# Kernel tuning notes

Hardware: AMD Instinct MI355X
Metric: run time of the kernel (lower is better)

## Reference

```python
import jax, jax.numpy as jnp
import numpy as np

def setup_inputs() -> dict:
    key = jax.random.key(0)
    k1, k2 = jax.random.split(key)
    B, T = 256, 100000
    x = jax.random.normal(k1, (B, T), dtype=jnp.float32)
    shifts = jax.random.randint(k2, (B,), 0, 1000, dtype=jnp.int32)
    return {"x": x, "shifts": shifts}

def reference(x, shifts):
    # tf.roll(x[i], shift=s, axis=0): out[j] = x[(j - s) % T]
    B, T = x.shape
    idx = (jnp.arange(T, dtype=jnp.int32)[None, :] - shifts[:, None]) % T  # [B, T]
    return jnp.take_along_axis(x, idx, axis=1)
```

## Files before the change

kernel.cpp:

```cpp
#include <hip/hip_runtime.h>

__global__ void roll_rows_vec4(const float* __restrict__ x,
                               const int* __restrict__ shifts,
                               float* __restrict__ out,
                               int T, int T4) {
    const int b = blockIdx.y;
    const int v = blockIdx.x * blockDim.x + threadIdx.x;
    if (v >= T4) return;

    int s = shifts[b] % T;
    if (s < 0) s += T;

    const int j = v * 4;
    int i0 = j - s;
    if (i0 < 0) i0 += T;

    const float* __restrict__ xr = x + (size_t)b * (size_t)T;
    float4 r;
    if (i0 + 3 < T) {
        r.x = xr[i0];
        r.y = xr[i0 + 1];
        r.z = xr[i0 + 2];
        r.w = xr[i0 + 3];
    } else {
        int i1 = i0 + 1; if (i1 >= T) i1 -= T;
        int i2 = i0 + 2; if (i2 >= T) i2 -= T;
        int i3 = i0 + 3; if (i3 >= T) i3 -= T;
        r.x = xr[i0];
        r.y = xr[i1];
        r.z = xr[i2];
        r.w = xr[i3];
    }
    *reinterpret_cast<float4*>(out + (size_t)b * (size_t)T + j) = r;
}

__global__ void roll_rows_scalar(const float* __restrict__ x,
                                 const int* __restrict__ shifts,
                                 float* __restrict__ out,
                                 int T) {
    const int b = blockIdx.y;
    const int j = blockIdx.x * blockDim.x + threadIdx.x;
    if (j >= T) return;
    int s = shifts[b] % T;
    if (s < 0) s += T;
    int i = j - s;
    if (i < 0) i += T;
    out[(size_t)b * T + j] = x[(size_t)b * T + i];
}

extern "C" void kernel_launch(void* const* d_in, const int* in_sizes, int n_in,
                              void* d_out, int out_size, void* d_ws, size_t ws_size,
                              hipStream_t stream) {
    const float* x = (const float*)d_in[0];
    const int* shifts = (const int*)d_in[1];
    float* out = (float*)d_out;

    const int B = in_sizes[1];
    const int T = in_sizes[0] / B;

    if ((T & 3) == 0) {
        const int T4 = T / 4;
        dim3 block(256);
        dim3 grid((T4 + 255) / 256, B);
        roll_rows_vec4<<<grid, block, 0, stream>>>(x, shifts, out, T, T4);
    } else {
        dim3 block(256);
        dim3 grid((T + 255) / 256, B);
        roll_rows_scalar<<<grid, block, 0, stream>>>(x, shifts, out, T);
    }
}
```

Baseline: 174.6 us.

## Stage rolled rows through padded LDS to use aligned float4 global loads

Replaces the per-thread scalar unaligned gathers with a block-level scheme. Each block reads an aligned span of the source row with float4 loads into padded shared memory, then reads it back at the shift offset and writes float4 outputs. The goal is fewer, wider global load transactions. In exchange it adds an LDS round trip and a barrier, and its correctness depends on T being a multiple of 4 so that the wrapped aligned loads stay in bounds.

```diff
diff --git a/kernel.cpp b/kernel.cpp
--- a/kernel.cpp
+++ b/kernel.cpp
@@ -1,37 +1,55 @@
 #include <hip/hip_runtime.h>
 
-__global__ void roll_rows_vec4(const float* __restrict__ x,
-                               const int* __restrict__ shifts,
-                               float* __restrict__ out,
-                               int T, int T4) {
+
+#define CHUNK 1024
+
+__device__ __forceinline__ int pad(int i) { return i + (i >> 2); }
+
+__global__ __launch_bounds__(256) void roll_rows_lds(
+    const float* __restrict__ x,
+    const int* __restrict__ shifts,
+    float* __restrict__ out,
+    int T) {
+    __shared__ float lds[CHUNK + 4 + ((CHUNK + 4) >> 2) + 4];
+
     const int b = blockIdx.y;
-    const int v = blockIdx.x * blockDim.x + threadIdx.x;
-    if (v >= T4) return;
+    const int chunk0 = blockIdx.x * CHUNK;
+    const int t = threadIdx.x;
 
     int s = shifts[b] % T;
     if (s < 0) s += T;
 
-    const int j = v * 4;
-    int i0 = j - s;
-    if (i0 < 0) i0 += T;
+    const int nOut = min(CHUNK, T - chunk0);
+    const int base = chunk0 - s;
+    const int off = ((base % 4) + 4) % 4;
+    const int baseAl = base - off;
+    const int nV = (nOut + off + 3) >> 2;
 
     const float* __restrict__ xr = x + (size_t)b * (size_t)T;
-    float4 r;
-    if (i0 + 3 < T) {
-        r.x = xr[i0];
-        r.y = xr[i0 + 1];
-        r.z = xr[i0 + 2];
-        r.w = xr[i0 + 3];
-    } else {
-        int i1 = i0 + 1; if (i1 >= T) i1 -= T;
-        int i2 = i0 + 2; if (i2 >= T) i2 -= T;
-        int i3 = i0 + 3; if (i3 >= T) i3 -= T;
-        r.x = xr[i0];
-        r.y = xr[i1];
-        r.z = xr[i2];
-        r.w = xr[i3];
+
+    for (int k = t; k < nV; k += 256) {
+        int src = baseAl + 4 * k;
+        if (src < 0) src += T;
+        else if (src >= T) src -= T;
+        const float4 v = *reinterpret_cast<const float4*>(xr + src);
+        const int i = 4 * k;
+        lds[pad(i + 0)] = v.x;
+        lds[pad(i + 1)] = v.y;
+        lds[pad(i + 2)] = v.z;
+        lds[pad(i + 3)] = v.w;
     }
-    *reinterpret_cast<float4*>(out + (size_t)b * (size_t)T + j) = r;
+    __syncthreads();
+
+    const int j = 4 * t;
+    if (j < nOut) {
+        const int i = off + j;
+        float4 o;
+        o.x = lds[pad(i + 0)];
+        o.y = lds[pad(i + 1)];
+        o.z = lds[pad(i + 2)];
+        o.w = lds[pad(i + 3)];
+        *reinterpret_cast<float4*>(out + (size_t)b * (size_t)T + chunk0 + j) = o;
+    }
 }
 
 __global__ void roll_rows_scalar(const float* __restrict__ x,
@@ -59,10 +77,9 @@
     const int T = in_sizes[0] / B;
 
     if ((T & 3) == 0) {
-        const int T4 = T / 4;
         dim3 block(256);
-        dim3 grid((T4 + 255) / 256, B);
-        roll_rows_vec4<<<grid, block, 0, stream>>>(x, shifts, out, T, T4);
+        dim3 grid((T + CHUNK - 1) / CHUNK, B);
+        roll_rows_lds<<<grid, block, 0, stream>>>(x, shifts, out, T);
     } else {
         dim3 block(256);
         dim3 grid((T + 255) / 256, B);
```

Result: no change. 177.8 us (+1.8%).

## Use aligned float4 loads with wavefront shuffle realignment for row roll

Applied to the files above, without the earlier changes.

Replaces the per-thread unaligned scalar gathers with a wave-per-chunk scheme. Each row is split into 32 spans, and each wavefront loads aligned float4 vectors. The misaligned offset is fixed with __shfl_down across lanes, so every lane writes a full float4 and 63 of 64 lanes store 252 floats per iteration. The change is meant to cut load instruction count and uncoalesced traffic on a bandwidth-bound copy. It adds shuffle overhead and one idle lane per wave, and it relies on blocks = B*32/4 dividing evenly.

```diff
diff --git a/kernel.cpp b/kernel.cpp
--- a/kernel.cpp
+++ b/kernel.cpp
@@ -1,37 +1,79 @@
 #include <hip/hip_runtime.h>
 
-__global__ void roll_rows_vec4(const float* __restrict__ x,
-                               const int* __restrict__ shifts,
-                               float* __restrict__ out,
-                               int T, int T4) {
-    const int b = blockIdx.y;
-    const int v = blockIdx.x * blockDim.x + threadIdx.x;
-    if (v >= T4) return;
 
-    int s = shifts[b] % T;
+#define WPR 32
+
+__global__ __launch_bounds__(256) void roll_rows_funnel(
+    const float* __restrict__ x,
+    const int* __restrict__ shifts,
+    float* __restrict__ out,
+    int T, int span) {
+    const int tid = blockIdx.x * 256 + threadIdx.x;
+    const int w = tid >> 6;
+    const int L = threadIdx.x & 63;
+    const int r = w / WPR;
+    const int k = w - r * WPR;
+
+    const int c0 = k * span;
+    if (c0 >= T) return;
+    const int len = min(span, T - c0);
+
+    int s = shifts[r] % T;
     if (s < 0) s += T;
 
-    const int j = v * 4;
-    int i0 = j - s;
-    if (i0 < 0) i0 += T;
+    const int base = c0 - s;
+    const int off = base & 3;
+    const int qb = base - off;
 
-    const float* __restrict__ xr = x + (size_t)b * (size_t)T;
-    float4 r;
-    if (i0 + 3 < T) {
-        r.x = xr[i0];
-        r.y = xr[i0 + 1];
-        r.z = xr[i0 + 2];
-        r.w = xr[i0 + 3];
+    const float* __restrict__ xr = x + (size_t)r * (size_t)T;
+    float* __restrict__ orow = out + (size_t)r * (size_t)T + c0;
+
+    const int iters = (len + 251) / 252;
+
+    if (off == 0) {
+        for (int i0 = 0; i0 < iters; i0 += 4) {
+            float4 q[4];
+#pragma unroll
+            for (int u = 0; u < 4; ++u) {
+                const int ii = min(i0 + u, iters - 1);
+                int src = qb + ii * 252 + 4 * L;
+                if (src < 0) src += T;
+                else if (src >= T) src -= T;
+                q[u] = *reinterpret_cast<const float4*>(xr + src);
+            }
+#pragma unroll
+            for (int u = 0; u < 4; ++u) {
+                const int jo = (i0 + u) * 252 + 4 * L;
+                if (L < 63 && jo < len)
+                    *reinterpret_cast<float4*>(orow + jo) = q[u];
+            }
+        }
     } else {
-        int i1 = i0 + 1; if (i1 >= T) i1 -= T;
-        int i2 = i0 + 2; if (i2 >= T) i2 -= T;
-        int i3 = i0 + 3; if (i3 >= T) i3 -= T;
-        r.x = xr[i0];
-        r.y = xr[i1];
-        r.z = xr[i2];
-        r.w = xr[i3];
+        for (int i0 = 0; i0 < iters; i0 += 4) {
+            float4 q[4];
+#pragma unroll
+            for (int u = 0; u < 4; ++u) {
+                const int ii = min(i0 + u, iters - 1);
+                int src = qb + ii * 252 + 4 * L;
+                if (src < 0) src += T;
+                else if (src >= T) src -= T;
+                q[u] = *reinterpret_cast<const float4*>(xr + src);
+            }
+#pragma unroll
+            for (int u = 0; u < 4; ++u) {
+                const float a0 = __shfl_down(q[u].x, 1, 64);
+                const float a1 = __shfl_down(q[u].y, 1, 64);
+                const float a2 = __shfl_down(q[u].z, 1, 64);
+                float4 rr;
+                if (off == 1)      rr = make_float4(q[u].y, q[u].z, q[u].w, a0);
+                else if (off == 2) rr = make_float4(q[u].z, q[u].w, a0, a1);
+                else               rr = make_float4(q[u].w, a0, a1, a2);
+                const int jo = (i0 + u) * 252 + 4 * L;
+                if (L < 63 && jo < len)
+                    *reinterpret_cast<float4*>(orow + jo) = rr;
+            }
+        }
     }
-    *reinterpret_cast<float4*>(out + (size_t)b * (size_t)T + j) = r;
 }
 
 __global__ void roll_rows_scalar(const float* __restrict__ x,
@@ -59,10 +101,10 @@
     const int T = in_sizes[0] / B;
 
     if ((T & 3) == 0) {
-        const int T4 = T / 4;
-        dim3 block(256);
-        dim3 grid((T4 + 255) / 256, B);
-        roll_rows_vec4<<<grid, block, 0, stream>>>(x, shifts, out, T, T4);
+        const int span = (((T + WPR - 1) / WPR) + 3) & ~3;
+        const int total_waves = B * WPR;
+        const int blocks = total_waves / 4;
+        roll_rows_funnel<<<blocks, 256, 0, stream>>>(x, shifts, out, T, span);
     } else {
         dim3 block(256);
         dim3 grid((T + 255) / 256, B);
```

Measured after the change: 191.2 us. 9.5% more time.
